# Kernel optimization log

Hardware: AMD Instinct MI355X
Metric: run time of the kernel (lower is better)

## Reference

```python
import jax, jax.numpy as jnp
import numpy as np

N_NODES = 100000
N_EDGES = 1600000
IN_FEATS = 128
OUT_FEATS = 128
K = 3
N_HEAD = 3


def setup_inputs() -> dict:
    key = jax.random.key(0)
    ks = jax.random.split(key, 8)
    feat = jax.random.normal(ks[0], (N_NODES, IN_FEATS), dtype=jnp.float32)
    stdv = 1.0 / np.sqrt(OUT_FEATS)
    fc_w = jax.random.uniform(ks[1], (OUT_FEATS, IN_FEATS), minval=-stdv, maxval=stdv, dtype=jnp.float32)
    fc_b = jnp.zeros((OUT_FEATS,), dtype=jnp.float32)
    stdvk = 1.0 / np.sqrt(K)
    alpha = jax.random.uniform(ks[2], (K + 1,), minval=-stdvk, maxval=stdvk, dtype=jnp.float32)
    stdh = 1.0 / np.sqrt(IN_FEATS)
    head_w = jax.random.uniform(ks[3], (N_HEAD, IN_FEATS), minval=-stdh, maxval=stdh, dtype=jnp.float32)
    head_b = jax.random.uniform(ks[4], (N_HEAD,), minval=-stdh, maxval=stdh, dtype=jnp.float32)
    src = jax.random.randint(ks[5], (N_EDGES,), 0, N_NODES, dtype=jnp.int32)
    dst = jax.random.randint(ks[6], (N_EDGES,), 0, N_NODES, dtype=jnp.int32)
    return {"feat": feat, "fc_w": fc_w, "fc_b": fc_b, "alpha": alpha,
            "head_w": head_w, "head_b": head_b, "src": src, "dst": dst}


def reference(feat, fc_w, fc_b, alpha, head_w, head_b, src, dst):
    # in-degree normalization: norm = clamp(in_deg, 1)^-0.5, shape [N,1]
    degs = jax.ops.segment_sum(jnp.ones_like(dst, dtype=jnp.float32), dst,
                               num_segments=N_NODES)
    norm = jnp.clip(degs, 1.0, None) ** -0.5
    norm = norm[:, None]

    # k-hop symmetric-normalized SpMM: h <- D^-1/2 A D^-1/2 h
    feat_list = [feat]
    h = feat
    for _ in range(K):
        h = h * norm
        h = jax.ops.segment_sum(h[src], dst, num_segments=N_NODES)  # copy_u/sum
        h = h * norm
        feat_list.append(h)
    feats = jnp.stack(feat_list, axis=0)  # [K+1, N, F]

    # per-head gating logits over hops: [H, N, K+1]
    logits = jnp.einsum('knf,hf->hnk', feats, head_w) + head_b[:, None, None]
    logp = jax.nn.log_softmax(logits, axis=-1)
    p = jnp.exp(logp)
    g = jnp.sum(p, axis=0)                      # [N, K+1] sum of head softmaxes
    entropy = -jnp.sum(p * logp, axis=(0, 2))   # [N] summed over heads

    # result = sum_i fc(feat_i * alpha_i * g_i); fc bias added K+1 times
    combined = jnp.einsum('kn,knf->nf', alpha[:, None] * g.T, feats)
    result = combined @ fc_w.T + (K + 1) * fc_b
    return result, entropy
```

## Files before the change

kernel.cpp:

```cpp
#include <hip/hip_runtime.h>
#include <hip/hip_fp16.h>

#define NF 128
#define NCHUNK 256
#define NBMAX 1024

typedef _Float16 f16x8 __attribute__((ext_vector_type(8)));
typedef float    f32x4 __attribute__((ext_vector_type(4)));

__global__ void k_histA(const int* __restrict__ dst, int* __restrict__ cnt, int n_edges, int epc,
                        const float* __restrict__ feat, __half* __restrict__ x0, int n8) {
    int bid = blockIdx.x;
    if (bid < NCHUNK) {
        __shared__ int h[NBMAX];
        for (int i = threadIdx.x; i < NBMAX; i += 256) h[i] = 0;
        __syncthreads();
        int e0 = bid * epc, e1 = min(e0 + epc, n_edges);
        for (int e = e0 + threadIdx.x; e < e1; e += 256)
            atomicAdd(&h[dst[e] >> 7], 1);
        __syncthreads();
        for (int i = threadIdx.x; i < NBMAX; i += 256)
            cnt[bid * NBMAX + i] = h[i];
    } else {
        int cb = bid - NCHUNK;
        const float4* f4 = reinterpret_cast<const float4*>(feat);
        for (int i8 = cb * 256 + threadIdx.x; i8 < n8; i8 += 512 * 256) {
            float4 v0 = f4[2 * i8];
            float4 v1 = f4[2 * i8 + 1];
            f16x8 o;
            o[0] = (_Float16)v0.x; o[1] = (_Float16)v0.y;
            o[2] = (_Float16)v0.z; o[3] = (_Float16)v0.w;
            o[4] = (_Float16)v1.x; o[5] = (_Float16)v1.y;
            o[6] = (_Float16)v1.z; o[7] = (_Float16)v1.w;
            reinterpret_cast<f16x8*>(x0)[i8] = o;
        }
    }
}

__global__ void k_redT(const int* __restrict__ cnt, int* __restrict__ T) {
    __shared__ int s[NCHUNK];
    int b = blockIdx.x;
    int tid = threadIdx.x;
    s[tid] = cnt[tid * NBMAX + b];
    __syncthreads();
    for (int o = NCHUNK / 2; o > 0; o >>= 1) {
        if (tid < o) s[tid] += s[tid + o];
        __syncthreads();
    }
    if (tid == 0) T[b] = s[0];
}

__global__ void k_scanT(const int* __restrict__ T, int* __restrict__ boff, int nb) {
    __shared__ int s[NBMAX];
    int tid = threadIdx.x;
    int v = (tid < nb) ? T[tid] : 0;
    s[tid] = v;
    __syncthreads();
    for (int o = 1; o < NBMAX; o <<= 1) {
        int t = (tid >= o) ? s[tid - o] : 0;
        __syncthreads();
        s[tid] += t;
        __syncthreads();
    }
    boff[tid] = s[tid] - v;
}

__global__ void k_chunkbase(int* __restrict__ cnt, const int* __restrict__ boff) {
    __shared__ int s[NCHUNK];
    int b = blockIdx.x;
    int tid = threadIdx.x;
    int v = cnt[tid * NBMAX + b];
    s[tid] = v;
    __syncthreads();
    for (int o = 1; o < NCHUNK; o <<= 1) {
        int t = (tid >= o) ? s[tid - o] : 0;
        __syncthreads();
        s[tid] += t;
        __syncthreads();
    }
    cnt[tid * NBMAX + b] = boff[b] + s[tid] - v;
}

__global__ void k_scatC(const int* __restrict__ src, const int* __restrict__ dst,
                        const int* __restrict__ cnt, int* __restrict__ buf,
                        int n_edges, int epc) {
    __shared__ int base[NBMAX];
    __shared__ int h2[NBMAX];
    int c = blockIdx.x;
    for (int i = threadIdx.x; i < NBMAX; i += 256) {
        base[i] = cnt[c * NBMAX + i];
        h2[i] = 0;
    }
    __syncthreads();
    int e0 = c * epc, e1 = min(e0 + epc, n_edges);
    for (int e = e0 + threadIdx.x; e < e1; e += 256) {
        int d = dst[e];
        int b = d >> 7;
        int idx = atomicAdd(&h2[b], 1);
        buf[base[b] + idx] = ((d & 127) << 17) | src[e];
    }
}

__global__ void k_bucketD(const int* __restrict__ buf, const int* __restrict__ T,
                          const int* __restrict__ boff, int* __restrict__ csr,
                          int* __restrict__ off, float* __restrict__ normv,
                          float* __restrict__ invnv, int n_nodes, int n_edges, int nb) {
    __shared__ int h[128], pb[128], h2[128];
    int b = blockIdx.x;
    int tid = threadIdx.x;
    if (tid < 128) h[tid] = 0;
    __syncthreads();
    int bo = boff[b];
    int tb = T[b];
    for (int e = bo + tid; e < bo + tb; e += 256)
        atomicAdd(&h[(buf[e] >> 17) & 127], 1);
    __syncthreads();
    int v = (tid < 128) ? h[tid] : 0;
    if (tid < 128) pb[tid] = v;
    __syncthreads();
    for (int o = 1; o < 128; o <<= 1) {
        int t = (tid < 128 && tid >= o) ? pb[tid - o] : 0;
        __syncthreads();
        if (tid < 128) pb[tid] += t;
        __syncthreads();
    }
    if (tid < 128) {
        int ex = pb[tid] - v;
        pb[tid] = bo + ex;
        int node = b * 128 + tid;
        if (node < n_nodes) {
            off[node] = bo + ex;
            int d = (v < 1) ? 1 : v;
            normv[node] = rsqrtf((float)d);
            invnv[node] = sqrtf((float)d);
        }
        h2[tid] = 0;
    }
    __syncthreads();
    if (b == nb - 1 && tid == 0) off[n_nodes] = n_edges;
    for (int e = bo + tid; e < bo + tb; e += 256) {
        int p = buf[e];
        int dl = (p >> 17) & 127;
        int pos = pb[dl] + atomicAdd(&h2[dl], 1);
        csr[pos] = p & 0x1FFFF;
    }
}

template<bool EDGE_SCALE>
__launch_bounds__(256)
__global__ void k_gather4(const __half* __restrict__ in, const int* __restrict__ csr,
                          const int* __restrict__ off, const float* __restrict__ normv,
                          __half* __restrict__ out, int n_nodes) {
    int wave = (blockIdx.x * blockDim.x + threadIdx.x) >> 6;
    int lane = threadIdx.x & 63;
    if (wave >= n_nodes) return;
    int e0 = off[wave], e1 = off[wave + 1];
    int g  = lane >> 4;
    int li = lane & 15;

    __half2 accA[4], accB[4];
#pragma unroll
    for (int j = 0; j < 4; ++j) {
        accA[j] = __half2half2(__float2half(0.f));
        accB[j] = __half2half2(__float2half(0.f));
    }

    const __half* inp = in + li * 8;
    int e = e0 + g;

    for (; e + 12 < e1; e += 16) {
        int sa = csr[e], sb = csr[e + 4], sc = csr[e + 8], sd = csr[e + 12];
        int4 ra = *reinterpret_cast<const int4*>(inp + (size_t)sa * NF);
        int4 rb = *reinterpret_cast<const int4*>(inp + (size_t)sb * NF);
        int4 rc = *reinterpret_cast<const int4*>(inp + (size_t)sc * NF);
        int4 rd = *reinterpret_cast<const int4*>(inp + (size_t)sd * NF);
        if (EDGE_SCALE) {
            __half2 fA = __float2half2_rn(normv[sa]);
            __half2 fB = __float2half2_rn(normv[sb]);
            __half2 fC = __float2half2_rn(normv[sc]);
            __half2 fD = __float2half2_rn(normv[sd]);
            accA[0] = __hfma2(__builtin_bit_cast(__half2, ra.x), fA, accA[0]);
            accA[1] = __hfma2(__builtin_bit_cast(__half2, ra.y), fA, accA[1]);
            accA[2] = __hfma2(__builtin_bit_cast(__half2, ra.z), fA, accA[2]);
            accA[3] = __hfma2(__builtin_bit_cast(__half2, ra.w), fA, accA[3]);
            accB[0] = __hfma2(__builtin_bit_cast(__half2, rb.x), fB, accB[0]);
            accB[1] = __hfma2(__builtin_bit_cast(__half2, rb.y), fB, accB[1]);
            accB[2] = __hfma2(__builtin_bit_cast(__half2, rb.z), fB, accB[2]);
            accB[3] = __hfma2(__builtin_bit_cast(__half2, rb.w), fB, accB[3]);
            accA[0] = __hfma2(__builtin_bit_cast(__half2, rc.x), fC, accA[0]);
            accA[1] = __hfma2(__builtin_bit_cast(__half2, rc.y), fC, accA[1]);
            accA[2] = __hfma2(__builtin_bit_cast(__half2, rc.z), fC, accA[2]);
            accA[3] = __hfma2(__builtin_bit_cast(__half2, rc.w), fC, accA[3]);
            accB[0] = __hfma2(__builtin_bit_cast(__half2, rd.x), fD, accB[0]);
            accB[1] = __hfma2(__builtin_bit_cast(__half2, rd.y), fD, accB[1]);
            accB[2] = __hfma2(__builtin_bit_cast(__half2, rd.z), fD, accB[2]);
            accB[3] = __hfma2(__builtin_bit_cast(__half2, rd.w), fD, accB[3]);
        } else {
            accA[0] = __hadd2(accA[0], __hadd2(__builtin_bit_cast(__half2, ra.x), __builtin_bit_cast(__half2, rc.x)));
            accA[1] = __hadd2(accA[1], __hadd2(__builtin_bit_cast(__half2, ra.y), __builtin_bit_cast(__half2, rc.y)));
            accA[2] = __hadd2(accA[2], __hadd2(__builtin_bit_cast(__half2, ra.z), __builtin_bit_cast(__half2, rc.z)));
            accA[3] = __hadd2(accA[3], __hadd2(__builtin_bit_cast(__half2, ra.w), __builtin_bit_cast(__half2, rc.w)));
            accB[0] = __hadd2(accB[0], __hadd2(__builtin_bit_cast(__half2, rb.x), __builtin_bit_cast(__half2, rd.x)));
            accB[1] = __hadd2(accB[1], __hadd2(__builtin_bit_cast(__half2, rb.y), __builtin_bit_cast(__half2, rd.y)));
            accB[2] = __hadd2(accB[2], __hadd2(__builtin_bit_cast(__half2, rb.z), __builtin_bit_cast(__half2, rd.z)));
            accB[3] = __hadd2(accB[3], __hadd2(__builtin_bit_cast(__half2, rb.w), __builtin_bit_cast(__half2, rd.w)));
        }
    }
    for (; e + 4 < e1; e += 8) {
        int sa = csr[e], sb = csr[e + 4];
        int4 ra = *reinterpret_cast<const int4*>(inp + (size_t)sa * NF);
        int4 rb = *reinterpret_cast<const int4*>(inp + (size_t)sb * NF);
        if (EDGE_SCALE) {
            __half2 fA = __float2half2_rn(normv[sa]);
            __half2 fB = __float2half2_rn(normv[sb]);
            accA[0] = __hfma2(__builtin_bit_cast(__half2, ra.x), fA, accA[0]);
            accA[1] = __hfma2(__builtin_bit_cast(__half2, ra.y), fA, accA[1]);
            accA[2] = __hfma2(__builtin_bit_cast(__half2, ra.z), fA, accA[2]);
            accA[3] = __hfma2(__builtin_bit_cast(__half2, ra.w), fA, accA[3]);
            accB[0] = __hfma2(__builtin_bit_cast(__half2, rb.x), fB, accB[0]);
            accB[1] = __hfma2(__builtin_bit_cast(__half2, rb.y), fB, accB[1]);
            accB[2] = __hfma2(__builtin_bit_cast(__half2, rb.z), fB, accB[2]);
            accB[3] = __hfma2(__builtin_bit_cast(__half2, rb.w), fB, accB[3]);
        } else {
            accA[0] = __hadd2(accA[0], __builtin_bit_cast(__half2, ra.x));
            accA[1] = __hadd2(accA[1], __builtin_bit_cast(__half2, ra.y));
            accA[2] = __hadd2(accA[2], __builtin_bit_cast(__half2, ra.z));
            accA[3] = __hadd2(accA[3], __builtin_bit_cast(__half2, ra.w));
            accB[0] = __hadd2(accB[0], __builtin_bit_cast(__half2, rb.x));
            accB[1] = __hadd2(accB[1], __builtin_bit_cast(__half2, rb.y));
            accB[2] = __hadd2(accB[2], __builtin_bit_cast(__half2, rb.z));
            accB[3] = __hadd2(accB[3], __builtin_bit_cast(__half2, rb.w));
        }
    }
    if (e < e1) {
        int sa = csr[e];
        int4 ra = *reinterpret_cast<const int4*>(inp + (size_t)sa * NF);
        if (EDGE_SCALE) {
            __half2 fA = __float2half2_rn(normv[sa]);
            accA[0] = __hfma2(__builtin_bit_cast(__half2, ra.x), fA, accA[0]);
            accA[1] = __hfma2(__builtin_bit_cast(__half2, ra.y), fA, accA[1]);
            accA[2] = __hfma2(__builtin_bit_cast(__half2, ra.z), fA, accA[2]);
            accA[3] = __hfma2(__builtin_bit_cast(__half2, ra.w), fA, accA[3]);
        } else {
            accA[0] = __hadd2(accA[0], __builtin_bit_cast(__half2, ra.x));
            accA[1] = __hadd2(accA[1], __builtin_bit_cast(__half2, ra.y));
            accA[2] = __hadd2(accA[2], __builtin_bit_cast(__half2, ra.z));
            accA[3] = __hadd2(accA[3], __builtin_bit_cast(__half2, ra.w));
        }
    }

    float fa[8];
#pragma unroll
    for (int j = 0; j < 4; ++j) {
        float2 f1 = __half22float2(accA[j]);
        float2 f2 = __half22float2(accB[j]);
        fa[2 * j] = f1.x + f2.x;
        fa[2 * j + 1] = f1.y + f2.y;
    }
#pragma unroll
    for (int j = 0; j < 8; ++j) {
        fa[j] += __shfl_xor(fa[j], 16, 64);
        fa[j] += __shfl_xor(fa[j], 32, 64);
    }
    if (g == 0) {
        float nv = normv[wave];
        float nn2 = nv * nv;
        f16x8 o;
#pragma unroll
        for (int j = 0; j < 8; ++j) o[j] = (_Float16)(fa[j] * nn2);
        *reinterpret_cast<f16x8*>(out + (size_t)wave * NF + li * 8) = o;
    }
}

__launch_bounds__(256)
__global__ void k_epi(const __half* __restrict__ x0, const __half* __restrict__ s1,
                      const __half* __restrict__ s2, const __half* __restrict__ s3,
                      const float* __restrict__ invnv,
                      const float* __restrict__ fc_w, const float* __restrict__ fc_b,
                      const float* __restrict__ alpha, const float* __restrict__ head_w,
                      const float* __restrict__ head_b,
                      float* __restrict__ out_res, float* __restrict__ out_ent, int n_nodes) {
    __shared__ _Float16 fcw[128 * 136];
    __shared__ float wlds[4][4][16];
    const int tid = threadIdx.x;
    const int lane = tid & 63;
    const int wid = tid >> 6;

    for (int i = 0; i < 16; ++i) {
        int idx = i * 1024 + tid * 4;
        int o = idx >> 7, f = idx & 127;
        float4 v = *reinterpret_cast<const float4*>(&fc_w[idx]);
        _Float16* p = &fcw[o * 136 + f];
        p[0] = (_Float16)v.x; p[1] = (_Float16)v.y;
        p[2] = (_Float16)v.z; p[3] = (_Float16)v.w;
    }
    __syncthreads();

    const int base = blockIdx.x * 64 + wid * 16;
    if (base + 16 > n_nodes) return;

    const int hi = lane >> 4;
    const int nx = lane & 15;

    f16x8 bh[4];
#pragma unroll
    for (int kt = 0; kt < 4; ++kt) {
#pragma unroll
        for (int j = 0; j < 8; ++j)
            bh[kt][j] = (nx < 3) ? (_Float16)head_w[nx * NF + kt * 32 + hi * 8 + j] : (_Float16)0.f;
    }

    const __half* xs[4] = {x0, s1, s2, s3};
    f16x8 a[4][4];
#pragma unroll
    for (int k = 0; k < 4; ++k) {
        const __half* xp = xs[k];
#pragma unroll
        for (int kt = 0; kt < 4; ++kt)
            a[k][kt] = *reinterpret_cast<const f16x8*>(xp + (size_t)(base + nx) * NF + kt * 32 + hi * 8);
    }

    f32x4 accL[4];
#pragma unroll
    for (int k = 0; k < 4; ++k) accL[k] = (f32x4){0.f, 0.f, 0.f, 0.f};
#pragma unroll
    for (int k = 0; k < 4; ++k)
#pragma unroll
        for (int kt = 0; kt < 4; ++kt)
            accL[k] = __builtin_amdgcn_mfma_f32_16x16x32_f16(a[k][kt], bh[kt], accL[k], 0, 0, 0);

    float4 in4 = *reinterpret_cast<const float4*>(&invnv[base + hi * 4]);
    float inr[4] = {in4.x, in4.y, in4.z, in4.w};
    float hb = (nx < 3) ? head_b[nx] : 0.f;
    float al0 = alpha[0], al1 = alpha[1], al2 = alpha[2], al3 = alpha[3];

#pragma unroll
    for (int r = 0; r < 4; ++r) {
        float ivx = inr[r];
        float l0 = accL[0][r] + hb;
        float l1 = fmaf(accL[1][r], ivx, hb);
        float l2 = fmaf(accL[2][r], ivx, hb);
        float l3 = fmaf(accL[3][r], ivx, hb);
        float mx = fmaxf(fmaxf(l0, l1), fmaxf(l2, l3));
        float e0 = __expf(l0 - mx), e1 = __expf(l1 - mx);
        float e2 = __expf(l2 - mx), e3 = __expf(l3 - mx);
        float s = e0 + e1 + e2 + e3;
        float inv = 1.f / s;
        float ls = __logf(s);
        float p0 = e0 * inv, p1 = e1 * inv, p2 = e2 * inv, p3 = e3 * inv;
        bool act = (nx < 3);
        float g0 = act ? p0 : 0.f, g1 = act ? p1 : 0.f;
        float g2 = act ? p2 : 0.f, g3 = act ? p3 : 0.f;
        float et = act ? -(p0 * (l0 - mx - ls) + p1 * (l1 - mx - ls) +
                           p2 * (l2 - mx - ls) + p3 * (l3 - mx - ls)) : 0.f;
        g0 += __shfl_xor(g0, 1, 64); g0 += __shfl_xor(g0, 2, 64);
        g1 += __shfl_xor(g1, 1, 64); g1 += __shfl_xor(g1, 2, 64);
        g2 += __shfl_xor(g2, 1, 64); g2 += __shfl_xor(g2, 2, 64);
        g3 += __shfl_xor(g3, 1, 64); g3 += __shfl_xor(g3, 2, 64);
        et += __shfl_xor(et, 1, 64); et += __shfl_xor(et, 2, 64);
        if (nx == 0) {
            int m = hi * 4 + r;
            wlds[wid][0][m] = al0 * g0;
            wlds[wid][1][m] = al1 * g1 * ivx;
            wlds[wid][2][m] = al2 * g2 * ivx;
            wlds[wid][3][m] = al3 * g3 * ivx;
            out_ent[base + m] = et;
        }
    }

    float ww0 = wlds[wid][0][nx];
    float ww1 = wlds[wid][1][nx];
    float ww2 = wlds[wid][2][nx];
    float ww3 = wlds[wid][3][nx];
    f16x8 ca[4];
#pragma unroll
    for (int kt = 0; kt < 4; ++kt) {
#pragma unroll
        for (int j = 0; j < 8; ++j) {
            float c = ww0 * (float)a[0][kt][j] + ww1 * (float)a[1][kt][j]
                    + ww2 * (float)a[2][kt][j] + ww3 * (float)a[3][kt][j];
            ca[kt][j] = (_Float16)c;
        }
    }

#pragma unroll
    for (int nt = 0; nt < 8; ++nt) {
        f32x4 acc = (f32x4){0.f, 0.f, 0.f, 0.f};
#pragma unroll
        for (int kt = 0; kt < 4; ++kt) {
            f16x8 b = *reinterpret_cast<const f16x8*>(&fcw[(nt * 16 + nx) * 136 + kt * 32 + hi * 8]);
            acc = __builtin_amdgcn_mfma_f32_16x16x32_f16(ca[kt], b, acc, 0, 0, 0);
        }
        float fcb4 = 4.f * fc_b[nt * 16 + nx];
#pragma unroll
        for (int r = 0; r < 4; ++r)
            out_res[(size_t)(base + hi * 4 + r) * NF + nt * 16 + nx] = acc[r] + fcb4;
    }
}

extern "C" void kernel_launch(void* const* d_in, const int* in_sizes, int n_in,
                              void* d_out, int out_size, void* d_ws, size_t ws_size,
                              hipStream_t stream) {
    const float* feat   = (const float*)d_in[0];
    const float* fc_w   = (const float*)d_in[1];
    const float* fc_b   = (const float*)d_in[2];
    const float* alpha  = (const float*)d_in[3];
    const float* head_w = (const float*)d_in[4];
    const float* head_b = (const float*)d_in[5];
    const int*   src    = (const int*)d_in[6];
    const int*   dst    = (const int*)d_in[7];

    const int N = in_sizes[0] / NF;
    const int E = in_sizes[6];
    const int nb = (N + 127) / 128;

    char* ws = (char*)d_ws;
    size_t pos = 0;
    auto alloc = [&](size_t bytes) -> char* {
        char* p = ws + pos;
        pos = (pos + bytes + 255) & ~(size_t)255;
        return p;
    };
    int*    cnt   = (int*)   alloc((size_t)NCHUNK * NBMAX * 4);
    int*    T     = (int*)   alloc((size_t)NBMAX * 4);
    int*    boff  = (int*)   alloc((size_t)NBMAX * 4);
    int*    buf   = (int*)   alloc((size_t)E * 4);
    int*    csr   = (int*)   alloc((size_t)E * 4);
    int*    off   = (int*)   alloc((size_t)(N + 1) * 4);
    float*  normv = (float*) alloc((size_t)N * 4);
    float*  invnv = (float*) alloc((size_t)N * 4);
    __half* x0    = (__half*)alloc((size_t)N * NF * 2);
    __half* s1    = (__half*)alloc((size_t)N * NF * 2);
    __half* s2    = (__half*)alloc((size_t)N * NF * 2);
    __half* s3    = (__half*)alloc((size_t)N * NF * 2);
    if (pos > ws_size) return;

    float* out_res = (float*)d_out;
    float* out_ent = out_res + (size_t)N * NF;

    const int epc = (E + NCHUNK - 1) / NCHUNK;
    const int n8  = N * NF / 8;

    k_histA    <<<NCHUNK + 512, 256, 0, stream>>>(dst, cnt, E, epc, feat, x0, n8);
    k_redT     <<<nb, NCHUNK, 0, stream>>>(cnt, T);
    k_scanT    <<<1, NBMAX, 0, stream>>>(T, boff, nb);
    k_chunkbase<<<nb, NCHUNK, 0, stream>>>(cnt, boff);
    k_scatC    <<<NCHUNK, 256, 0, stream>>>(src, dst, cnt, buf, E, epc);
    k_bucketD  <<<nb, 256, 0, stream>>>(buf, T, boff, csr, off, normv, invnv, N, E, nb);

    const int gb = (N * 64 + 255) / 256;
    k_gather4<true> <<<gb, 256, 0, stream>>>(x0, csr, off, normv, s1, N);
    k_gather4<false><<<gb, 256, 0, stream>>>(s1, csr, off, normv, s2, N);
    k_gather4<false><<<gb, 256, 0, stream>>>(s2, csr, off, normv, s3, N);

    const int eb = (N + 63) / 64;
    k_epi<<<eb, 256, 0, stream>>>(x0, s1, s2, s3, invnv, fc_w, fc_b,
                                  alpha, head_w, head_b, out_res, out_ent, N);
}
```

Baseline: 275.4 us.

## Fuse final SpMM hop into epilogue kernel, dropping s3 buffer

```diff
diff --git a/kernel.cpp b/kernel.cpp
--- a/kernel.cpp
+++ b/kernel.cpp
@@ -146,6 +146,61 @@
     }
 }
 
+__device__ __forceinline__ void gather_row_nosc(const __half* __restrict__ inp,
+                                                const int* __restrict__ csr,
+                                                int e0, int e1, int g, float* fa ) {
+    __half2 accA[4], accB[4];
+#pragma unroll
+    for (int j = 0; j < 4; ++j) {
+        accA[j] = __half2half2(__float2half(0.f));
+        accB[j] = __half2half2(__float2half(0.f));
+    }
+    int e = e0 + g;
+    for (; e + 12 < e1; e += 16) {
+        int sa = csr[e], sb = csr[e + 4], sc = csr[e + 8], sd = csr[e + 12];
+        int4 ra = *reinterpret_cast<const int4*>(inp + (size_t)sa * NF);
+        int4 rb = *reinterpret_cast<const int4*>(inp + (size_t)sb * NF);
+        int4 rc = *reinterpret_cast<const int4*>(inp + (size_t)sc * NF);
+        int4 rd = *reinterpret_cast<const int4*>(inp + (size_t)sd * NF);
+        accA[0] = __hadd2(accA[0], __hadd2(__builtin_bit_cast(__half2, ra.x), __builtin_bit_cast(__half2, rc.x)));
+        accA[1] = __hadd2(accA[1], __hadd2(__builtin_bit_cast(__half2, ra.y), __builtin_bit_cast(__half2, rc.y)));
+        accA[2] = __hadd2(accA[2], __hadd2(__builtin_bit_cast(__half2, ra.z), __builtin_bit_cast(__half2, rc.z)));
+        accA[3] = __hadd2(accA[3], __hadd2(__builtin_bit_cast(__half2, ra.w), __builtin_bit_cast(__half2, rc.w)));
+        accB[0] = __hadd2(accB[0], __hadd2(__builtin_bit_cast(__half2, rb.x), __builtin_bit_cast(__half2, rd.x)));
+        accB[1] = __hadd2(accB[1], __hadd2(__builtin_bit_cast(__half2, rb.y), __builtin_bit_cast(__half2, rd.y)));
+        accB[2] = __hadd2(accB[2], __hadd2(__builtin_bit_cast(__half2, rb.z), __builtin_bit_cast(__half2, rd.z)));
+        accB[3] = __hadd2(accB[3], __hadd2(__builtin_bit_cast(__half2, rb.w), __builtin_bit_cast(__half2, rd.w)));
+    }
+    for (; e + 4 < e1; e += 8) {
+        int sa = csr[e], sb = csr[e + 4];
+        int4 ra = *reinterpret_cast<const int4*>(inp + (size_t)sa * NF);
+        int4 rb = *reinterpret_cast<const int4*>(inp + (size_t)sb * NF);
+        accA[0] = __hadd2(accA[0], __builtin_bit_cast(__half2, ra.x));
+        accA[1] = __hadd2(accA[1], __builtin_bit_cast(__half2, ra.y));
+        accA[2] = __hadd2(accA[2], __builtin_bit_cast(__half2, ra.z));
+        accA[3] = __hadd2(accA[3], __builtin_bit_cast(__half2, ra.w));
+        accB[0] = __hadd2(accB[0], __builtin_bit_cast(__half2, rb.x));
+        accB[1] = __hadd2(accB[1], __builtin_bit_cast(__half2, rb.y));
+        accB[2] = __hadd2(accB[2], __builtin_bit_cast(__half2, rb.z));
+        accB[3] = __hadd2(accB[3], __builtin_bit_cast(__half2, rb.w));
+    }
+    if (e < e1) {
+        int sa = csr[e];
+        int4 ra = *reinterpret_cast<const int4*>(inp + (size_t)sa * NF);
+        accA[0] = __hadd2(accA[0], __builtin_bit_cast(__half2, ra.x));
+        accA[1] = __hadd2(accA[1], __builtin_bit_cast(__half2, ra.y));
+        accA[2] = __hadd2(accA[2], __builtin_bit_cast(__half2, ra.z));
+        accA[3] = __hadd2(accA[3], __builtin_bit_cast(__half2, ra.w));
+    }
+#pragma unroll
+    for (int j = 0; j < 4; ++j) {
+        float2 f1 = __half22float2(accA[j]);
+        float2 f2 = __half22float2(accB[j]);
+        fa[2 * j] = f1.x + f2.x;
+        fa[2 * j + 1] = f1.y + f2.y;
+    }
+}
+
 template<bool EDGE_SCALE>
 __launch_bounds__(256)
 __global__ void k_gather4(const __half* __restrict__ in, const int* __restrict__ csr,
@@ -157,24 +212,23 @@
     int e0 = off[wave], e1 = off[wave + 1];
     int g  = lane >> 4;
     int li = lane & 15;
-
-    __half2 accA[4], accB[4];
-#pragma unroll
-    for (int j = 0; j < 4; ++j) {
-        accA[j] = __half2half2(__float2half(0.f));
-        accB[j] = __half2half2(__float2half(0.f));
-    }
-
     const __half* inp = in + li * 8;
-    int e = e0 + g;
-
-    for (; e + 12 < e1; e += 16) {
-        int sa = csr[e], sb = csr[e + 4], sc = csr[e + 8], sd = csr[e + 12];
-        int4 ra = *reinterpret_cast<const int4*>(inp + (size_t)sa * NF);
-        int4 rb = *reinterpret_cast<const int4*>(inp + (size_t)sb * NF);
-        int4 rc = *reinterpret_cast<const int4*>(inp + (size_t)sc * NF);
-        int4 rd = *reinterpret_cast<const int4*>(inp + (size_t)sd * NF);
-        if (EDGE_SCALE) {
+
+    float fa[8];
+    if (EDGE_SCALE) {
+        __half2 accA[4], accB[4];
+#pragma unroll
+        for (int j = 0; j < 4; ++j) {
+            accA[j] = __half2half2(__float2half(0.f));
+            accB[j] = __half2half2(__float2half(0.f));
+        }
+        int e = e0 + g;
+        for (; e + 12 < e1; e += 16) {
+            int sa = csr[e], sb = csr[e + 4], sc = csr[e + 8], sd = csr[e + 12];
+            int4 ra = *reinterpret_cast<const int4*>(inp + (size_t)sa * NF);
+            int4 rb = *reinterpret_cast<const int4*>(inp + (size_t)sb * NF);
+            int4 rc = *reinterpret_cast<const int4*>(inp + (size_t)sc * NF);
+            int4 rd = *reinterpret_cast<const int4*>(inp + (size_t)sd * NF);
             __half2 fA = __float2half2_rn(normv[sa]);
             __half2 fB = __float2half2_rn(normv[sb]);
             __half2 fC = __float2half2_rn(normv[sc]);
@@ -195,68 +249,27 @@
             accB[1] = __hfma2(__builtin_bit_cast(__half2, rd.y), fD, accB[1]);
             accB[2] = __hfma2(__builtin_bit_cast(__half2, rd.z), fD, accB[2]);
             accB[3] = __hfma2(__builtin_bit_cast(__half2, rd.w), fD, accB[3]);
-        } else {
-            accA[0] = __hadd2(accA[0], __hadd2(__builtin_bit_cast(__half2, ra.x), __builtin_bit_cast(__half2, rc.x)));
-            accA[1] = __hadd2(accA[1], __hadd2(__builtin_bit_cast(__half2, ra.y), __builtin_bit_cast(__half2, rc.y)));
-            accA[2] = __hadd2(accA[2], __hadd2(__builtin_bit_cast(__half2, ra.z), __builtin_bit_cast(__half2, rc.z)));
-            accA[3] = __hadd2(accA[3], __hadd2(__builtin_bit_cast(__half2, ra.w), __builtin_bit_cast(__half2, rc.w)));
-            accB[0] = __hadd2(accB[0], __hadd2(__builtin_bit_cast(__half2, rb.x), __builtin_bit_cast(__half2, rd.x)));
-            accB[1] = __hadd2(accB[1], __hadd2(__builtin_bit_cast(__half2, rb.y), __builtin_bit_cast(__half2, rd.y)));
-            accB[2] = __hadd2(accB[2], __hadd2(__builtin_bit_cast(__half2, rb.z), __builtin_bit_cast(__half2, rd.z)));
-            accB[3] = __hadd2(accB[3], __hadd2(__builtin_bit_cast(__half2, rb.w), __builtin_bit_cast(__half2, rd.w)));
-        }
-    }
-    for (; e + 4 < e1; e += 8) {
-        int sa = csr[e], sb = csr[e + 4];
-        int4 ra = *reinterpret_cast<const int4*>(inp + (size_t)sa * NF);
-        int4 rb = *reinterpret_cast<const int4*>(inp + (size_t)sb * NF);
-        if (EDGE_SCALE) {
-            __half2 fA = __float2half2_rn(normv[sa]);
-            __half2 fB = __float2half2_rn(normv[sb]);
-            accA[0] = __hfma2(__builtin_bit_cast(__half2, ra.x), fA, accA[0]);
-            accA[1] = __hfma2(__builtin_bit_cast(__half2, ra.y), fA, accA[1]);
-            accA[2] = __hfma2(__builtin_bit_cast(__half2, ra.z), fA, accA[2]);
-            accA[3] = __hfma2(__builtin_bit_cast(__half2, ra.w), fA, accA[3]);
-            accB[0] = __hfma2(__builtin_bit_cast(__half2, rb.x), fB, accB[0]);
-            accB[1] = __hfma2(__builtin_bit_cast(__half2, rb.y), fB, accB[1]);
-            accB[2] = __hfma2(__builtin_bit_cast(__half2, rb.z), fB, accB[2]);
-            accB[3] = __hfma2(__builtin_bit_cast(__half2, rb.w), fB, accB[3]);
-        } else {
-            accA[0] = __hadd2(accA[0], __builtin_bit_cast(__half2, ra.x));
-            accA[1] = __hadd2(accA[1], __builtin_bit_cast(__half2, ra.y));
-            accA[2] = __hadd2(accA[2], __builtin_bit_cast(__half2, ra.z));
-            accA[3] = __hadd2(accA[3], __builtin_bit_cast(__half2, ra.w));
-            accB[0] = __hadd2(accB[0], __builtin_bit_cast(__half2, rb.x));
-            accB[1] = __hadd2(accB[1], __builtin_bit_cast(__half2, rb.y));
-            accB[2] = __hadd2(accB[2], __builtin_bit_cast(__half2, rb.z));
-            accB[3] = __hadd2(accB[3], __builtin_bit_cast(__half2, rb.w));
-        }
-    }
-    if (e < e1) {
-        int sa = csr[e];
-        int4 ra = *reinterpret_cast<const int4*>(inp + (size_t)sa * NF);
-        if (EDGE_SCALE) {
+        }
+        for (; e < e1; e += 4) {
+            int sa = csr[e];
+            int4 ra = *reinterpret_cast<const int4*>(inp + (size_t)sa * NF);
             __half2 fA = __float2half2_rn(normv[sa]);
             accA[0] = __hfma2(__builtin_bit_cast(__half2, ra.x), fA, accA[0]);
             accA[1] = __hfma2(__builtin_bit_cast(__half2, ra.y), fA, accA[1]);
             accA[2] = __hfma2(__builtin_bit_cast(__half2, ra.z), fA, accA[2]);
             accA[3] = __hfma2(__builtin_bit_cast(__half2, ra.w), fA, accA[3]);
-        } else {
-            accA[0] = __hadd2(accA[0], __builtin_bit_cast(__half2, ra.x));
-            accA[1] = __hadd2(accA[1], __builtin_bit_cast(__half2, ra.y));
-            accA[2] = __hadd2(accA[2], __builtin_bit_cast(__half2, ra.z));
-            accA[3] = __hadd2(accA[3], __builtin_bit_cast(__half2, ra.w));
-        }
-    }
-
-    float fa[8];
-#pragma unroll
-    for (int j = 0; j < 4; ++j) {
-        float2 f1 = __half22float2(accA[j]);
-        float2 f2 = __half22float2(accB[j]);
-        fa[2 * j] = f1.x + f2.x;
-        fa[2 * j + 1] = f1.y + f2.y;
-    }
+        }
+#pragma unroll
+        for (int j = 0; j < 4; ++j) {
+            float2 f1 = __half22float2(accA[j]);
+            float2 f2 = __half22float2(accB[j]);
+            fa[2 * j] = f1.x + f2.x;
+            fa[2 * j + 1] = f1.y + f2.y;
+        }
+    } else {
+        gather_row_nosc(inp, csr, e0, e1, g, fa);
+    }
+
 #pragma unroll
     for (int j = 0; j < 8; ++j) {
         fa[j] += __shfl_xor(fa[j], 16, 64);
@@ -273,14 +286,16 @@
 }
 
 __launch_bounds__(256)
-__global__ void k_epi(const __half* __restrict__ x0, const __half* __restrict__ s1,
-                      const __half* __restrict__ s2, const __half* __restrict__ s3,
-                      const float* __restrict__ invnv,
-                      const float* __restrict__ fc_w, const float* __restrict__ fc_b,
-                      const float* __restrict__ alpha, const float* __restrict__ head_w,
-                      const float* __restrict__ head_b,
-                      float* __restrict__ out_res, float* __restrict__ out_ent, int n_nodes) {
+__global__ void k_gepi(const __half* __restrict__ x0, const __half* __restrict__ s1,
+                       const __half* __restrict__ s2,
+                       const int* __restrict__ csr, const int* __restrict__ off,
+                       const float* __restrict__ normv, const float* __restrict__ invnv,
+                       const float* __restrict__ fc_w, const float* __restrict__ fc_b,
+                       const float* __restrict__ alpha, const float* __restrict__ head_w,
+                       const float* __restrict__ head_b,
+                       float* __restrict__ out_res, float* __restrict__ out_ent, int n_nodes) {
     __shared__ _Float16 fcw[128 * 136];
+    __shared__ _Float16 srow[4][16][136];
     __shared__ float wlds[4][4][16];
     const int tid = threadIdx.x;
     const int lane = tid & 63;
@@ -301,6 +316,28 @@
 
     const int hi = lane >> 4;
     const int nx = lane & 15;
+    const int g  = lane >> 4;
+    const int li = lane & 15;
+
+    const __half* inp = s2 + li * 8;
+    for (int j = 0; j < 16; ++j) {
+        int n = base + j;
+        float fa[8];
+        gather_row_nosc(inp, csr, off[n], off[n + 1], g, fa);
+#pragma unroll
+        for (int q = 0; q < 8; ++q) {
+            fa[q] += __shfl_xor(fa[q], 16, 64);
+            fa[q] += __shfl_xor(fa[q], 32, 64);
+        }
+        if (g == 0) {
+            float nv = normv[n];
+            float nn2 = nv * nv;
+            f16x8 o;
+#pragma unroll
+            for (int q = 0; q < 8; ++q) o[q] = (_Float16)(fa[q] * nn2);
+            *reinterpret_cast<f16x8*>(&srow[wid][j][li * 8]) = o;
+        }
+    }
 
     f16x8 bh[4];
 #pragma unroll
@@ -310,15 +347,18 @@
             bh[kt][j] = (nx < 3) ? (_Float16)head_w[nx * NF + kt * 32 + hi * 8 + j] : (_Float16)0.f;
     }
 
-    const __half* xs[4] = {x0, s1, s2, s3};
+    const __half* xs[3] = {x0, s1, s2};
     f16x8 a[4][4];
 #pragma unroll
-    for (int k = 0; k < 4; ++k) {
+    for (int k = 0; k < 3; ++k) {
         const __half* xp = xs[k];
 #pragma unroll
         for (int kt = 0; kt < 4; ++kt)
             a[k][kt] = *reinterpret_cast<const f16x8*>(xp + (size_t)(base + nx) * NF + kt * 32 + hi * 8);
     }
+#pragma unroll
+    for (int kt = 0; kt < 4; ++kt)
+        a[3][kt] = *reinterpret_cast<const f16x8*>(&srow[wid][nx][kt * 32 + hi * 8]);
 
     f32x4 accL[4];
 #pragma unroll
@@ -432,7 +472,6 @@
     __half* x0    = (__half*)alloc((size_t)N * NF * 2);
     __half* s1    = (__half*)alloc((size_t)N * NF * 2);
     __half* s2    = (__half*)alloc((size_t)N * NF * 2);
-    __half* s3    = (__half*)alloc((size_t)N * NF * 2);
     if (pos > ws_size) return;
 
     float* out_res = (float*)d_out;
@@ -451,9 +490,8 @@
     const int gb = (N * 64 + 255) / 256;
     k_gather4<true> <<<gb, 256, 0, stream>>>(x0, csr, off, normv, s1, N);
     k_gather4<false><<<gb, 256, 0, stream>>>(s1, csr, off, normv, s2, N);
-    k_gather4<false><<<gb, 256, 0, stream>>>(s2, csr, off, normv, s3, N);
 
     const int eb = (N + 63) / 64;
-    k_epi<<<eb, 256, 0, stream>>>(x0, s1, s2, s3, invnv, fc_w, fc_b,
-                                  alpha, head_w, head_b, out_res, out_ent, N);
-}
+    k_gepi<<<eb, 256, 0, stream>>>(x0, s1, s2, csr, off, normv, invnv, fc_w, fc_b,
+                                   alpha, head_w, head_b, out_res, out_ent, N);
+}
```

Result: slower. 340.2 us (+23.5%).
